# Performance work log

Hardware: AMD Instinct MI355X
Metric: run time of the kernel (lower is better)

## Reference

```python
import jax, jax.numpy as jnp
import numpy as np

K_WIN = 7  # temporal window size (odd)
EPS = 1e-5


def setup_inputs() -> dict:
    key = jax.random.key(0)
    ks = jax.random.split(key, 10)
    B, C, T, H, W = 8, 512, 32, 7, 7
    N, E = 8, 64  # heads, inter channels = C // N
    s = 0.02
    return {
        "x": jax.random.normal(ks[0], (B, C, T, H, W), jnp.float32),
        "gamma": jnp.ones((C,), jnp.float32),
        "beta": jnp.zeros((C,), jnp.float32),
        "Wq": jax.random.normal(ks[1], (N, E, C), jnp.float32) * s,
        "bq": jax.random.normal(ks[2], (N, E), jnp.float32) * s,
        "Wk": jax.random.normal(ks[3], (N, E, C), jnp.float32) * s,
        "bk": jax.random.normal(ks[4], (N, E), jnp.float32) * s,
        "Wv": jax.random.normal(ks[5], (N, E, C), jnp.float32) * s,
        "bv": jax.random.normal(ks[6], (N, E), jnp.float32) * s,
        "Wo": jax.random.normal(ks[7], (N, C, E), jnp.float32) * s,
        "bo": jax.random.normal(ks[8], (N, C), jnp.float32) * s,
    }


def reference(x, gamma, beta, Wq, bq, Wk, bk, Wv, bv, Wo, bo):
    B, C, T, H, W = x.shape
    K = K_WIN
    P = H * W          # spatial positions per frame
    L = K * P          # positions per temporal window

    # BatchNorm3d (training-mode batch stats over B,T,H,W)
    mean = jnp.mean(x, axis=(0, 2, 3, 4), keepdims=True)
    var = jnp.var(x, axis=(0, 2, 3, 4), keepdims=True)
    g = gamma[None, :, None, None, None]
    b = beta[None, :, None, None, None]
    xb = g * (x - mean) * jax.lax.rsqrt(var + EPS) + b  # (B,C,T,H,W)

    # temporal zero-pad so that number of windows S == T
    pad = K // 2
    xp = jnp.pad(xb, ((0, 0), (0, 0), (pad, pad), (0, 0), (0, 0)))
    # gather sliding windows: (B,C,T,K,H,W)
    win_idx = jnp.arange(T)[:, None] + jnp.arange(K)[None, :]
    xw = xp[:, :, win_idx]

    xwf = xw.reshape(B, C, T, L)   # window tokens (key/value source)
    xcf = xb.reshape(B, C, T, P)   # center frame (query source)

    # per-head projections (dropout is identity in eval mode)
    q = jnp.einsum('nec,bctp->bntep', Wq, xcf) + bq[None, :, None, :, None]
    k = jnp.einsum('nec,bctl->bntel', Wk, xwf) + bk[None, :, None, :, None]
    v = jnp.einsum('nec,bctl->bntel', Wv, xwf) + bv[None, :, None, :, None]

    # attention: scores (B,N,T,P,L), softmax over window positions L (no scaling, as in original)
    alpha = jnp.einsum('bntep,bntel->bntpl', q, k)
    alpha = jax.nn.softmax(alpha, axis=-1)
    y = jnp.einsum('bntpl,bntel->bntep', alpha, v)

    # output projection per head, then mean over heads
    out = jnp.einsum('nce,bntep->bntcp', Wo, y) + bo[None, :, None, :, None]
    z = jnp.mean(out, axis=1)                 # (B,T,C,P)
    z = jnp.transpose(z, (0, 2, 1, 3)).reshape(B, C, T, H, W)
    return z + xb  # residual with BN output
```

## Files before the change

kernel.cpp:

```cpp
#include <hip/hip_runtime.h>
#include <hip/hip_bf16.h>


typedef float f32x4 __attribute__((ext_vector_type(4)));
typedef short s16x8 __attribute__((ext_vector_type(8)));
typedef short s16x4 __attribute__((ext_vector_type(4)));
typedef __bf16 bf16x8 __attribute__((ext_vector_type(8)));

static __device__ __forceinline__ float bf2f(unsigned short u){
  union { unsigned int i; float f; } x; x.i = ((unsigned int)u) << 16; return x.f;
}
static __device__ __forceinline__ unsigned short f2bf(float f){
  union { __hip_bfloat16 h; unsigned short u; } x; x.h = __float2bfloat16(f); return x.u;
}
static __device__ __forceinline__ f32x4 mfma16(s16x8 a, s16x8 b, f32x4 c){
  return __builtin_amdgcn_mfma_f32_16x16x32_bf16(
      __builtin_bit_cast(bf16x8, a), __builtin_bit_cast(bf16x8, b), c, 0, 0, 0);
}
static __device__ __forceinline__ void gload16(const unsigned short* g, unsigned short* l){
  __builtin_amdgcn_global_load_lds(
      (const __attribute__((address_space(1))) unsigned int*)g,
      (__attribute__((address_space(3))) unsigned int*)l, 16, 0, 0);
}

__global__ __launch_bounds__(256) void stats_kernel(const float* __restrict__ x,
    const float* __restrict__ gamma, const float* __restrict__ beta,
    float* __restrict__ scale, float* __restrict__ shift){
  const int c = blockIdx.x, tid = threadIdx.x;
  float s1 = 0.f, s2 = 0.f;
  const float* xc = x + (size_t)c*1568;
  for (int i = tid; i < 3136; i += 256){
    int b = i / 392, j = i - b*392;
    f32x4 v = *(const f32x4*)(xc + (size_t)b*802816 + j*4);
    s1 += v[0]+v[1]+v[2]+v[3];
    s2 += v[0]*v[0]+v[1]*v[1]+v[2]*v[2]+v[3]*v[3];
  }
  #pragma unroll
  for (int off = 32; off > 0; off >>= 1){
    s1 += __shfl_down(s1, off);
    s2 += __shfl_down(s2, off);
  }
  __shared__ float r1[4], r2[4];
  int wave = tid >> 6, lane = tid & 63;
  if (lane == 0){ r1[wave] = s1; r2[wave] = s2; }
  __syncthreads();
  if (tid == 0){
    float t1 = r1[0]+r1[1]+r1[2]+r1[3];
    float t2 = r2[0]+r2[1]+r2[2]+r2[3];
    const float inv = 1.f/12544.f;
    float mean = t1*inv;
    float var  = t2*inv - mean*mean;
    float sc = gamma[c]*rsqrtf(var + 1e-5f);
    scale[c] = sc;
    shift[c] = beta[c] - mean*sc;
  }
}

__global__ __launch_bounds__(512) void pack_kernel(const float* __restrict__ Wq,
    const float* __restrict__ Wk, const float* __restrict__ Wv,
    const float* __restrict__ Wo, const float* __restrict__ bo,
    unsigned short* __restrict__ Wall, unsigned short* __restrict__ Wo2,
    float* __restrict__ bo_sum){
  int i = blockIdx.x*512 + threadIdx.x;
  if (i < 786432){
    const float* W = (i < 262144) ? Wq : (i < 524288 ? Wk : Wv);
    Wall[i] = f2bf(W[i & 262143]);
  } else if (i < 1048576){
    int j = i - 786432;
    int c = j >> 9, k = j & 511, nn = k >> 6, e = k & 63;
    Wo2[j] = f2bf(Wo[((size_t)nn*512 + c)*64 + e] * 0.125f);
  } else if (i < 1049088){
    int c = i - 1048576;
    float s = 0.f;
    #pragma unroll
    for (int nn = 0; nn < 8; ++nn) s += bo[nn*512 + c];
    bo_sum[c] = s * 0.125f;
  }
}

__global__ __launch_bounds__(256) void xt_kernel(const float* __restrict__ x,
    const float* __restrict__ scale, const float* __restrict__ shift,
    unsigned short* __restrict__ Xt){
  __shared__ unsigned short Xc[512][52];
  const int bt = blockIdx.x, b = bt >> 5, t = bt & 31, tid = threadIdx.x;
  const float* xb = x + (size_t)b*802816 + t*49;
  for (int i = tid; i < 512*49; i += 256){
    int c = i / 49, p = i - c*49;
    Xc[c][p] = f2bf(xb[(size_t)c*1568 + p]*scale[c] + shift[c]);
  }
  __syncthreads();
  unsigned short* dst = Xt + (size_t)bt*32768;
  for (int i = tid; i < 4096; i += 256){
    int p = i & 63, c0 = (i >> 6) << 3;
    s16x8 v;
    #pragma unroll
    for (int j = 0; j < 8; ++j) v[j] = (p < 49) ? (short)Xc[c0+j][p] : (short)0;
    *(s16x8*)(dst + p*512 + c0) = v;
  }
}

__global__ __launch_bounds__(256) void qkv_gemm(const unsigned short* __restrict__ Wall,
    const unsigned short* __restrict__ Xt,
    const float* __restrict__ bq, const float* __restrict__ bk, const float* __restrict__ bv,
    unsigned short* __restrict__ Qg, unsigned short* __restrict__ Kg,
    unsigned short* __restrict__ Vg){
  __shared__ unsigned short As[2][4096];
  __shared__ unsigned short Bs[2][4096];
  const int bid = blockIdx.x;
  const int id = (bid & 7)*192 + (bid >> 3);
  const int bm = id % 12, bn = id / 12;
  const int m0 = bm*128, n0 = bn*128;
  const int tid = threadIdx.x;
  const int w = __builtin_amdgcn_readfirstlane(tid >> 6);
  const int lane = tid & 63, l15 = lane & 15, g = lane >> 4, g4 = (lane >> 4)*4;
  const int wm = w >> 1, wn = w & 1;
  const int cA = w*128 + lane;
  int offA[4], offB[4];
  #pragma unroll
  for (int mi = 0; mi < 4; ++mi){
    int row = wm*64 + mi*16 + l15;
    offA[mi] = row*32 + ((g ^ ((row>>1)&3))<<3);
  }
  #pragma unroll
  for (int ni = 0; ni < 4; ++ni){
    int col = wn*64 + ni*16 + l15;
    offB[ni] = col*32 + ((g ^ ((col>>1)&3))<<3);
  }
  f32x4 acc[4][4];
  #pragma unroll
  for (int mi = 0; mi < 4; ++mi)
    #pragma unroll
    for (int ni = 0; ni < 4; ++ni) acc[mi][ni] = 0.f;

  auto stage = [&](int bufi, int ks){
    #pragma unroll
    for (int it = 0; it < 2; ++it){
      int c = cA + it*64;
      int row = c >> 2, slot = c & 3;
      int ko = ks*32 + ((slot ^ ((row>>1)&3))<<3);
      gload16(Wall + (size_t)(m0 + row)*512 + ko, &As[bufi][(w*128 + it*64)*8]);
      gload16(Xt   + (size_t)(n0 + row)*512 + ko, &Bs[bufi][(w*128 + it*64)*8]);
    }
  };
  auto compute = [&](int bufi){
    s16x8 Af[4], Bf[4];
    #pragma unroll
    for (int mi = 0; mi < 4; ++mi) Af[mi] = *(const s16x8*)&As[bufi][offA[mi]];
    #pragma unroll
    for (int ni = 0; ni < 4; ++ni) Bf[ni] = *(const s16x8*)&Bs[bufi][offB[ni]];
    #pragma unroll
    for (int mi = 0; mi < 4; ++mi)
      #pragma unroll
      for (int ni = 0; ni < 4; ++ni)
        acc[mi][ni] = mfma16(Af[mi], Bf[ni], acc[mi][ni]);
  };

  stage(0, 0);
  __syncthreads();
  #pragma unroll 1
  for (int kk = 0; kk < 8; ++kk){
    stage(1, kk*2 + 1);
    compute(0);
    __syncthreads();
    if (kk < 7) stage(0, kk*2 + 2);
    compute(1);
    __syncthreads();
  }

  const int qb = bm*2 + wm;
  const int which = qb >> 3, n = qb & 7;
  const int bt = bn*2 + wn, b = bt >> 5, t = bt & 31;
  const size_t bnt = ((size_t)(b*8 + n)*32 + t);
  const float* bias = which == 0 ? bq : (which == 1 ? bk : bv);
  #pragma unroll
  for (int mi = 0; mi < 4; ++mi){
    const int e0 = mi*16 + g4;
    const f32x4 bb = *(const f32x4*)(bias + n*64 + e0);
    #pragma unroll
    for (int ni = 0; ni < 4; ++ni){
      const int p = ni*16 + l15;
      f32x4 v = acc[mi][ni] + bb;
      if (which == 0) v *= 1.4426950408889634f;
      if (p < 49){
        if (which < 2){
          s16x4 u;
          #pragma unroll
          for (int r = 0; r < 4; ++r) u[r] = (short)f2bf(v[r]);
          *(s16x4*)((which == 0 ? Qg : Kg) + (bnt*49 + p)*64 + e0) = u;
        } else {
          #pragma unroll
          for (int r = 0; r < 4; ++r)
            Vg[bnt*3328 + (size_t)(e0 + r)*52 + p] = f2bf(v[r]);
        }
      }
    }
  }
}

__global__ __launch_bounds__(512,2) void attn_kernel(const unsigned short* __restrict__ Qg,
    const unsigned short* __restrict__ Kg, const unsigned short* __restrict__ Vg,
    const float* __restrict__ bk, const float* __restrict__ bv,
    unsigned short* __restrict__ Yg){
  const int bid = blockIdx.x;
  const int bt = ((bid & 7) << 5) | (bid >> 3);
  const int b = bt >> 5, t = bt & 31, tid = threadIdx.x;
  const int n = __builtin_amdgcn_readfirstlane(tid >> 6);
  const int lane = tid & 63, g = lane >> 4, l15 = lane & 15, g4 = (lane >> 4)*4;
  const size_t bnt = ((size_t)(b*8 + n)*32 + t);
  const unsigned short* Qb = Qg + bnt*3136;
  s16x8 Qf[4][2];
  #pragma unroll
  for (int ni = 0; ni < 4; ++ni)
    #pragma unroll
    for (int ks = 0; ks < 2; ++ks)
      Qf[ni][ks] = *(const s16x8*)(Qb + (ni*16 + l15)*64 + ks*32 + g*8);
  const float* bkp = bk + n*64;
  f32x4 bkf[2][2];
  bkf[0][0] = *(const f32x4*)(bkp + g*8);      bkf[0][1] = *(const f32x4*)(bkp + g*8 + 4);
  bkf[1][0] = *(const f32x4*)(bkp + 32 + g*8); bkf[1][1] = *(const f32x4*)(bkp + 32 + g*8 + 4);
  float pad_l[4];
  #pragma unroll
  for (int ni = 0; ni < 4; ++ni){
    float s = 0.f;
    #pragma unroll
    for (int ks = 0; ks < 2; ++ks)
      #pragma unroll
      for (int h = 0; h < 2; ++h)
        #pragma unroll
        for (int j = 0; j < 4; ++j)
          s += bf2f((unsigned short)Qf[ni][ks][h*4+j]) * bkf[ks][h][j];
    s += __shfl_xor(s, 16); s += __shfl_xor(s, 32);
    pad_l[ni] = s;
  }
  float m_run[4], d_run[4];
  f32x4 Yacc[4][4];
  #pragma unroll
  for (int ni = 0; ni < 4; ++ni){
    m_run[ni] = -1e30f; d_run[ni] = 0.f;
    #pragma unroll
    for (int me = 0; me < 4; ++me) Yacc[me][ni] = 0.f;
  }
  int slo = 3 - t; if (slo < 0) slo = 0;
  int shi = 34 - t; if (shi > 6) shi = 6;
  for (int s = slo; s <= shi; ++s){
    const int tt = t + s - 3;
    const unsigned short* Kb = Kg + ((size_t)(b*8 + n)*32 + tt)*3136;
    const unsigned short* Vb = Vg + ((size_t)(b*8 + n)*32 + tt)*3328;
    f32x4 S[4][4];
    #pragma unroll
    for (int mi = 0; mi < 4; ++mi)
      #pragma unroll
      for (int ni = 0; ni < 4; ++ni) S[mi][ni] = 0.f;
    __builtin_amdgcn_s_setprio(1);
    #pragma unroll
    for (int ks = 0; ks < 2; ++ks)
      #pragma unroll
      for (int mi = 0; mi < 4; ++mi){
        s16x8 Kf = *(const s16x8*)(Kb + (mi*16 + l15)*64 + ks*32 + g*8);
        #pragma unroll
        for (int ni = 0; ni < 4; ++ni)
          S[mi][ni] = mfma16(Kf, Qf[ni][ks], S[mi][ni]);
      }
    __builtin_amdgcn_s_setprio(0);
    #pragma unroll
    for (int r = 0; r < 4; ++r){
      const bool bad = (g4 + r) >= 1;
      #pragma unroll
      for (int ni = 0; ni < 4; ++ni)
        S[3][ni][r] = bad ? -1e30f : S[3][ni][r];
    }
    #pragma unroll
    for (int ni = 0; ni < 4; ++ni){
      float mx = -1e30f;
      #pragma unroll
      for (int mi = 0; mi < 4; ++mi)
        #pragma unroll
        for (int r = 0; r < 4; ++r) mx = fmaxf(mx, S[mi][ni][r]);
      mx = fmaxf(mx, __shfl_xor(mx, 16));
      mx = fmaxf(mx, __shfl_xor(mx, 32));
      const float mn = fmaxf(m_run[ni], mx);
      const float rs = exp2f(m_run[ni] - mn);
      m_run[ni] = mn;
      float sum = 0.f;
      #pragma unroll
      for (int mi = 0; mi < 4; ++mi)
        #pragma unroll
        for (int r = 0; r < 4; ++r){
          float e = exp2f(S[mi][ni][r] - mn);
          S[mi][ni][r] = e; sum += e;
        }
      sum += __shfl_xor(sum, 16); sum += __shfl_xor(sum, 32);
      d_run[ni] = d_run[ni]*rs + sum;
      #pragma unroll
      for (int me = 0; me < 4; ++me) Yacc[me][ni] *= rs;
    }
    #pragma unroll
    for (int ks = 0; ks < 2; ++ks){
      s16x8 Pf[4];
      #pragma unroll
      for (int ni = 0; ni < 4; ++ni){
        f32x4 a = S[2*ks][ni], b2 = S[2*ks+1][ni];
        s16x8 pf;
        #pragma unroll
        for (int j = 0; j < 4; ++j){
          pf[j]   = (short)f2bf(a[j]);
          pf[4+j] = (short)f2bf(b2[j]);
        }
        Pf[ni] = pf;
      }
      __builtin_amdgcn_s_setprio(1);
      #pragma unroll
      for (int me = 0; me < 4; ++me){
        s16x4 vlo = *(const s16x4*)(Vb + (size_t)(me*16 + l15)*52 + ks*32 + g4);
        s16x4 vhi = *(const s16x4*)(Vb + (size_t)(me*16 + l15)*52 + ks*32 + 16 + g4);
        s16x8 Vf;
        #pragma unroll
        for (int j = 0; j < 4; ++j){ Vf[j] = vlo[j]; Vf[4+j] = vhi[j]; }
        #pragma unroll
        for (int ni = 0; ni < 4; ++ni)
          Yacc[me][ni] = mfma16(Vf, Pf[ni], Yacc[me][ni]);
      }
      __builtin_amdgcn_s_setprio(0);
    }
  }
  const int n_pad = slo + (6 - shi);
  f32x4 bvf[4];
  #pragma unroll
  for (int me = 0; me < 4; ++me)
    bvf[me] = *(const f32x4*)(bv + n*64 + me*16 + g4);
  unsigned short* Yb = Yg + bnt*3136;
  #pragma unroll
  for (int ni = 0; ni < 4; ++ni){
    float rs = 1.f, pw = 0.f, d = d_run[ni];
    if (n_pad > 0){
      const float mf = fmaxf(m_run[ni], pad_l[ni]);
      rs = exp2f(m_run[ni] - mf);
      pw = (float)(n_pad*49) * exp2f(pad_l[ni] - mf);
      d = d_run[ni]*rs + pw;
    }
    const float inv = 1.f/d;
    const int p = ni*16 + l15;
    if (p < 49){
      #pragma unroll
      for (int me = 0; me < 4; ++me){
        s16x4 u;
        #pragma unroll
        for (int r = 0; r < 4; ++r)
          u[r] = (short)f2bf((Yacc[me][ni][r]*rs + pw*bvf[me][r])*inv);
        *(s16x4*)(Yb + (size_t)p*64 + me*16 + g4) = u;
      }
    }
  }
}

__global__ __launch_bounds__(256) void out_gemm(const unsigned short* __restrict__ Wo2,
    const unsigned short* __restrict__ Yg, const unsigned short* __restrict__ Xt,
    const float* __restrict__ scale, const float* __restrict__ shift,
    const float* __restrict__ bo_sum, float* __restrict__ out){
  __shared__ unsigned short As[2][4096];
  __shared__ unsigned short Bs[2][4096];
  const int bid = blockIdx.x;
  const int id = (bid & 7)*64 + (bid >> 3);
  const int bm = id % 4, bn = id / 4;
  const int m0 = bm*128, n0 = bn*128;
  const int tid = threadIdx.x;
  const int w = __builtin_amdgcn_readfirstlane(tid >> 6);
  const int lane = tid & 63, l15 = lane & 15, g = lane >> 4, g4 = (lane >> 4)*4;
  const int wm = w >> 1, wn = w & 1;
  const int cA = w*128 + lane;
  int offA[4], offB[4];
  #pragma unroll
  for (int mi = 0; mi < 4; ++mi){
    int row = wm*64 + mi*16 + l15;
    offA[mi] = row*32 + ((g ^ ((row>>1)&3))<<3);
  }
  #pragma unroll
  for (int ni = 0; ni < 4; ++ni){
    int col = wn*64 + ni*16 + l15;
    offB[ni] = col*32 + ((g ^ ((col>>1)&3))<<3);
  }
  f32x4 acc[4][4];
  #pragma unroll
  for (int mi = 0; mi < 4; ++mi)
    #pragma unroll
    for (int ni = 0; ni < 4; ++ni) acc[mi][ni] = 0.f;

  auto stage = [&](int bufi, int ks){
    const int nh = ks >> 1, eo = (ks & 1)*32;
    #pragma unroll
    for (int it = 0; it < 2; ++it){
      int c = cA + it*64;
      int row = c >> 2, slot = c & 3;
      int sw = ((slot ^ ((row>>1)&3))<<3);
      gload16(Wo2 + (size_t)(m0 + row)*512 + ks*32 + sw, &As[bufi][(w*128 + it*64)*8]);
      const int col = n0 + row, btc = col >> 6, p = col & 63;
      const size_t bb = ((size_t)((btc >> 5)*8 + nh)*32 + (btc & 31));
      gload16(Yg + bb*3136 + p*64 + eo + sw, &Bs[bufi][(w*128 + it*64)*8]);
    }
  };
  auto compute = [&](int bufi){
    s16x8 Af[4], Bf[4];
    #pragma unroll
    for (int mi = 0; mi < 4; ++mi) Af[mi] = *(const s16x8*)&As[bufi][offA[mi]];
    #pragma unroll
    for (int ni = 0; ni < 4; ++ni) Bf[ni] = *(const s16x8*)&Bs[bufi][offB[ni]];
    #pragma unroll
    for (int mi = 0; mi < 4; ++mi)
      #pragma unroll
      for (int ni = 0; ni < 4; ++ni)
        acc[mi][ni] = mfma16(Af[mi], Bf[ni], acc[mi][ni]);
  };

  stage(0, 0);
  __syncthreads();
  #pragma unroll 1
  for (int kk = 0; kk < 8; ++kk){
    stage(1, kk*2 + 1);
    compute(0);
    __syncthreads();
    if (kk < 7) stage(0, kk*2 + 2);
    compute(1);
    __syncthreads();
  }

  const int cb = m0 + wm*64;
  const int bt = bn*2 + wn, b = bt >> 5, t = bt & 31;
  const unsigned short* XtB = Xt + (size_t)bt*32768;
  #pragma unroll
  for (int mi = 0; mi < 4; ++mi){
    const int c0 = cb + mi*16 + g4;
    const f32x4 sc = *(const f32x4*)(bo_sum + c0);
    #pragma unroll
    for (int ni = 0; ni < 4; ++ni){
      const int p = ni*16 + l15;
      if (p < 49){
        s16x4 xb = *(const s16x4*)(XtB + p*512 + c0);
        #pragma unroll
        for (int r = 0; r < 4; ++r){
          const int c = c0 + r;
          out[((size_t)(b*512 + c))*1568 + t*49 + p] =
              acc[mi][ni][r] + sc[r] + bf2f((unsigned short)xb[r]);
        }
      }
    }
  }
}

extern "C" void kernel_launch(void* const* d_in, const int* in_sizes, int n_in_,
                              void* d_out, int out_size, void* d_ws, size_t ws_size,
                              hipStream_t stream){
  const float* x     = (const float*)d_in[0];
  const float* gamma = (const float*)d_in[1];
  const float* beta  = (const float*)d_in[2];
  const float* Wq    = (const float*)d_in[3];
  const float* bq    = (const float*)d_in[4];
  const float* Wk    = (const float*)d_in[5];
  const float* bk    = (const float*)d_in[6];
  const float* Wv    = (const float*)d_in[7];
  const float* bv    = (const float*)d_in[8];
  const float* Wo    = (const float*)d_in[9];
  const float* bo    = (const float*)d_in[10];
  float* out = (float*)d_out;

  char* ws = (char*)d_ws;
  float* scale  = (float*)ws;
  float* shift  = scale + 512;
  float* bo_sum = shift + 512;
  unsigned short* Wall = (unsigned short*)(ws + 8192);
  const size_t PAD = 16384;
  unsigned short* Wo2 = Wall + 786432;
  unsigned short* Xt  = Wo2 + 262144;
  unsigned short* Qg  = Xt + 8388608;
  unsigned short* Kg  = Qg + 6422528 + PAD;
  unsigned short* Vg  = Kg + 6422528 + PAD;
  unsigned short* Yg  = Vg + 6815744 + PAD;

  hipLaunchKernelGGL(stats_kernel, dim3(512), dim3(256), 0, stream,
                     x, gamma, beta, scale, shift);
  hipLaunchKernelGGL(pack_kernel, dim3(2049), dim3(512), 0, stream,
                     Wq, Wk, Wv, Wo, bo, Wall, Wo2, bo_sum);
  hipLaunchKernelGGL(xt_kernel, dim3(256), dim3(256), 0, stream,
                     x, scale, shift, Xt);
  hipLaunchKernelGGL(qkv_gemm, dim3(1536), dim3(256), 0, stream,
                     Wall, Xt, bq, bk, bv, Qg, Kg, Vg);
  hipLaunchKernelGGL(attn_kernel, dim3(256), dim3(512), 0, stream,
                     Qg, Kg, Vg, bk, bv, Yg);
  hipLaunchKernelGGL(out_gemm, dim3(512), dim3(256), 0, stream,
                     Wo2, Yg, Xt, scale, shift, bo_sum, out);
}
```

Measured before the change: 128.4 us.

## Deepen GEMM LDS pipeline to four stages with vmcnt-based waits

Both the QKV and output-projection GEMMs move from a double-buffered LDS pipeline synchronised by __syncthreads to a four-buffer ring. The ring prefetches three k-steps ahead and waits with explicit s_waitcnt vmcnt plus a raw s_barrier, so global loads stay in flight across iterations instead of being drained every step. The compute phase also runs under raised wave priority. In exchange LDS use per block doubles to 64 KB, which may cut occupancy, and the hand-counted vmcnt values must match the number of loads issued per stage.

```diff
diff --git a/kernel.cpp b/kernel.cpp
--- a/kernel.cpp
+++ b/kernel.cpp
@@ -22,6 +22,7 @@
       (const __attribute__((address_space(1))) unsigned int*)g,
       (__attribute__((address_space(3))) unsigned int*)l, 16, 0, 0);
 }
+#define VMCNT(N) asm volatile("s_waitcnt vmcnt(" #N ")" ::: "memory")
 
 __global__ __launch_bounds__(256) void stats_kernel(const float* __restrict__ x,
     const float* __restrict__ gamma, const float* __restrict__ beta,
@@ -104,8 +105,8 @@
     const float* __restrict__ bq, const float* __restrict__ bk, const float* __restrict__ bv,
     unsigned short* __restrict__ Qg, unsigned short* __restrict__ Kg,
     unsigned short* __restrict__ Vg){
-  __shared__ unsigned short As[2][4096];
-  __shared__ unsigned short Bs[2][4096];
+  __shared__ unsigned short As[4][4096];
+  __shared__ unsigned short Bs[4][4096];
   const int bid = blockIdx.x;
   const int id = (bid & 7)*192 + (bid >> 3);
   const int bm = id % 12, bn = id / 12;
@@ -155,17 +156,23 @@
         acc[mi][ni] = mfma16(Af[mi], Bf[ni], acc[mi][ni]);
   };
 
-  stage(0, 0);
-  __syncthreads();
+  stage(0, 0); stage(1, 1); stage(2, 2);
   #pragma unroll 1
-  for (int kk = 0; kk < 8; ++kk){
-    stage(1, kk*2 + 1);
-    compute(0);
-    __syncthreads();
-    if (kk < 7) stage(0, kk*2 + 2);
-    compute(1);
-    __syncthreads();
-  }
+  for (int j = 0; j < 13; ++j){
+    VMCNT(8);
+    __builtin_amdgcn_s_barrier();
+    __builtin_amdgcn_sched_barrier(0);
+    stage((j+3) & 3, j+3);
+    __builtin_amdgcn_s_setprio(1);
+    compute(j & 3);
+    __builtin_amdgcn_s_setprio(0);
+  }
+  VMCNT(8);  __builtin_amdgcn_s_barrier(); __builtin_amdgcn_sched_barrier(0);
+  __builtin_amdgcn_s_setprio(1); compute(1); __builtin_amdgcn_s_setprio(0);
+  VMCNT(4);  __builtin_amdgcn_s_barrier(); __builtin_amdgcn_sched_barrier(0);
+  __builtin_amdgcn_s_setprio(1); compute(2); __builtin_amdgcn_s_setprio(0);
+  VMCNT(0);  __builtin_amdgcn_s_barrier(); __builtin_amdgcn_sched_barrier(0);
+  __builtin_amdgcn_s_setprio(1); compute(3); __builtin_amdgcn_s_setprio(0);
 
   const int qb = bm*2 + wm;
   const int which = qb >> 3, n = qb & 7;
@@ -357,8 +364,8 @@
     const unsigned short* __restrict__ Yg, const unsigned short* __restrict__ Xt,
     const float* __restrict__ scale, const float* __restrict__ shift,
     const float* __restrict__ bo_sum, float* __restrict__ out){
-  __shared__ unsigned short As[2][4096];
-  __shared__ unsigned short Bs[2][4096];
+  __shared__ unsigned short As[4][4096];
+  __shared__ unsigned short Bs[4][4096];
   const int bid = blockIdx.x;
   const int id = (bid & 7)*64 + (bid >> 3);
   const int bm = id % 4, bn = id / 4;
@@ -411,17 +418,23 @@
         acc[mi][ni] = mfma16(Af[mi], Bf[ni], acc[mi][ni]);
   };
 
-  stage(0, 0);
-  __syncthreads();
+  stage(0, 0); stage(1, 1); stage(2, 2);
   #pragma unroll 1
-  for (int kk = 0; kk < 8; ++kk){
-    stage(1, kk*2 + 1);
-    compute(0);
-    __syncthreads();
-    if (kk < 7) stage(0, kk*2 + 2);
-    compute(1);
-    __syncthreads();
-  }
+  for (int j = 0; j < 13; ++j){
+    VMCNT(8);
+    __builtin_amdgcn_s_barrier();
+    __builtin_amdgcn_sched_barrier(0);
+    stage((j+3) & 3, j+3);
+    __builtin_amdgcn_s_setprio(1);
+    compute(j & 3);
+    __builtin_amdgcn_s_setprio(0);
+  }
+  VMCNT(8);  __builtin_amdgcn_s_barrier(); __builtin_amdgcn_sched_barrier(0);
+  __builtin_amdgcn_s_setprio(1); compute(1); __builtin_amdgcn_s_setprio(0);
+  VMCNT(4);  __builtin_amdgcn_s_barrier(); __builtin_amdgcn_sched_barrier(0);
+  __builtin_amdgcn_s_setprio(1); compute(2); __builtin_amdgcn_s_setprio(0);
+  VMCNT(0);  __builtin_amdgcn_s_barrier(); __builtin_amdgcn_sched_barrier(0);
+  __builtin_amdgcn_s_setprio(1); compute(3); __builtin_amdgcn_s_setprio(0);
 
   const int cb = m0 + wm*64;
   const int bt = bn*2 + wn, b = bt >> 5, t = bt & 31;
```

Result: no change. 130.7 us (+1.7%).

## Fold BatchNorm into QKV weights and pack tokens densely without padding

Applied to the files above, without the earlier changes.

Raw x is now transposed to bf16 once, and the BN statistics are computed from that bf16 copy in a two-pass reduction instead of a strided read of x. The BN scale is folded into the QKV weights and the shift into per-row biases, and the normalized residual is rebuilt in the out_gemm epilogue. Token columns are packed densely (49 per frame instead of padded to 64), which shrinks the QKV and output GEMM grids and removes wasted MFMA work. This adds two small kernels and computes the statistics from bf16-rounded values, a slight change in precision.

```diff
diff --git a/kernel.cpp b/kernel.cpp
--- a/kernel.cpp
+++ b/kernel.cpp
@@ -3,6 +3,7 @@
 
 
 typedef float f32x4 __attribute__((ext_vector_type(4)));
+typedef float f32x2 __attribute__((ext_vector_type(2)));
 typedef short s16x8 __attribute__((ext_vector_type(8)));
 typedef short s16x4 __attribute__((ext_vector_type(4)));
 typedef __bf16 bf16x8 __attribute__((ext_vector_type(8)));
@@ -23,48 +24,80 @@
       (__attribute__((address_space(3))) unsigned int*)l, 16, 0, 0);
 }
 
-__global__ __launch_bounds__(256) void stats_kernel(const float* __restrict__ x,
+__global__ __launch_bounds__(256) void xt_kernel(const float* __restrict__ x,
+    unsigned short* __restrict__ Xt){
+  __shared__ unsigned short Xc[512][53];
+  const int bt = blockIdx.x, b = bt >> 5, t = bt & 31, tid = threadIdx.x;
+  const float* xb = x + (size_t)b*802816 + t*49;
+  for (int i = tid; i < 512*49; i += 256){
+    int c = i / 49, p = i - c*49;
+    Xc[c][p] = f2bf(xb[(size_t)c*1568 + p]);
+  }
+  __syncthreads();
+  unsigned short* dst = Xt + (size_t)bt*49*512;
+  for (int i = tid; i < 49*64; i += 256){
+    int p = i >> 6, c0 = (i & 63) << 3;
+    s16x8 v;
+    #pragma unroll
+    for (int j = 0; j < 8; ++j) v[j] = (short)Xc[c0+j][p];
+    *(s16x8*)(dst + p*512 + c0) = v;
+  }
+}
+
+__global__ __launch_bounds__(256) void stats1_kernel(const unsigned short* __restrict__ Xt,
+    float* __restrict__ partials){
+  __shared__ float R1[4][512];
+  __shared__ float R2[4][512];
+  const int blk = blockIdx.x, tid = threadIdx.x;
+  const int rt = tid >> 6, c0 = (tid & 63)*8;
+  const int r0 = blk*128;
+  float s1[8] = {0,0,0,0,0,0,0,0}, s2[8] = {0,0,0,0,0,0,0,0};
+  for (int r = rt; r < 128; r += 4){
+    s16x8 v = *(const s16x8*)(Xt + (size_t)(r0 + r)*512 + c0);
+    #pragma unroll
+    for (int j = 0; j < 8; ++j){
+      float f = bf2f((unsigned short)v[j]);
+      s1[j] += f; s2[j] += f*f;
+    }
+  }
+  #pragma unroll
+  for (int j = 0; j < 8; ++j){ R1[rt][c0+j] = s1[j]; R2[rt][c0+j] = s2[j]; }
+  __syncthreads();
+  for (int c = tid; c < 512; c += 256){
+    f32x2 o;
+    o[0] = R1[0][c]+R1[1][c]+R1[2][c]+R1[3][c];
+    o[1] = R2[0][c]+R2[1][c]+R2[2][c]+R2[3][c];
+    *(f32x2*)(partials + ((size_t)blk*512 + c)*2) = o;
+  }
+}
+
+__global__ __launch_bounds__(512) void stats2_kernel(const float* __restrict__ partials,
     const float* __restrict__ gamma, const float* __restrict__ beta,
     float* __restrict__ scale, float* __restrict__ shift){
-  const int c = blockIdx.x, tid = threadIdx.x;
+  const int c = threadIdx.x;
   float s1 = 0.f, s2 = 0.f;
-  const float* xc = x + (size_t)c*1568;
-  for (int i = tid; i < 3136; i += 256){
-    int b = i / 392, j = i - b*392;
-    f32x4 v = *(const f32x4*)(xc + (size_t)b*802816 + j*4);
-    s1 += v[0]+v[1]+v[2]+v[3];
-    s2 += v[0]*v[0]+v[1]*v[1]+v[2]*v[2]+v[3]*v[3];
-  }
-  #pragma unroll
-  for (int off = 32; off > 0; off >>= 1){
-    s1 += __shfl_down(s1, off);
-    s2 += __shfl_down(s2, off);
-  }
-  __shared__ float r1[4], r2[4];
-  int wave = tid >> 6, lane = tid & 63;
-  if (lane == 0){ r1[wave] = s1; r2[wave] = s2; }
-  __syncthreads();
-  if (tid == 0){
-    float t1 = r1[0]+r1[1]+r1[2]+r1[3];
-    float t2 = r2[0]+r2[1]+r2[2]+r2[3];
-    const float inv = 1.f/12544.f;
-    float mean = t1*inv;
-    float var  = t2*inv - mean*mean;
-    float sc = gamma[c]*rsqrtf(var + 1e-5f);
-    scale[c] = sc;
-    shift[c] = beta[c] - mean*sc;
-  }
+  for (int k = 0; k < 98; ++k){
+    f32x2 v = *(const f32x2*)(partials + ((size_t)k*512 + c)*2);
+    s1 += v[0]; s2 += v[1];
+  }
+  const float inv = 1.f/12544.f;
+  float mean = s1*inv;
+  float var  = s2*inv - mean*mean;
+  float sc = gamma[c]*rsqrtf(var + 1e-5f);
+  scale[c] = sc;
+  shift[c] = beta[c] - mean*sc;
 }
 
 __global__ __launch_bounds__(512) void pack_kernel(const float* __restrict__ Wq,
     const float* __restrict__ Wk, const float* __restrict__ Wv,
     const float* __restrict__ Wo, const float* __restrict__ bo,
+    const float* __restrict__ scale,
     unsigned short* __restrict__ Wall, unsigned short* __restrict__ Wo2,
     float* __restrict__ bo_sum){
   int i = blockIdx.x*512 + threadIdx.x;
   if (i < 786432){
     const float* W = (i < 262144) ? Wq : (i < 524288 ? Wk : Wv);
-    Wall[i] = f2bf(W[i & 262143]);
+    Wall[i] = f2bf(W[i & 262143] * scale[i & 511]);
   } else if (i < 1048576){
     int j = i - 786432;
     int c = j >> 9, k = j & 511, nn = k >> 6, e = k & 63;
@@ -78,36 +111,32 @@
   }
 }
 
-__global__ __launch_bounds__(256) void xt_kernel(const float* __restrict__ x,
-    const float* __restrict__ scale, const float* __restrict__ shift,
-    unsigned short* __restrict__ Xt){
-  __shared__ unsigned short Xc[512][52];
-  const int bt = blockIdx.x, b = bt >> 5, t = bt & 31, tid = threadIdx.x;
-  const float* xb = x + (size_t)b*802816 + t*49;
-  for (int i = tid; i < 512*49; i += 256){
-    int c = i / 49, p = i - c*49;
-    Xc[c][p] = f2bf(xb[(size_t)c*1568 + p]*scale[c] + shift[c]);
-  }
-  __syncthreads();
-  unsigned short* dst = Xt + (size_t)bt*32768;
-  for (int i = tid; i < 4096; i += 256){
-    int p = i & 63, c0 = (i >> 6) << 3;
-    s16x8 v;
-    #pragma unroll
-    for (int j = 0; j < 8; ++j) v[j] = (p < 49) ? (short)Xc[c0+j][p] : (short)0;
-    *(s16x8*)(dst + p*512 + c0) = v;
-  }
+__global__ __launch_bounds__(64) void bias_kernel(const float* __restrict__ Wq,
+    const float* __restrict__ Wk, const float* __restrict__ Wv,
+    const float* __restrict__ bq, const float* __restrict__ bk,
+    const float* __restrict__ bv, const float* __restrict__ shift,
+    float* __restrict__ biasAll){
+  const int row = blockIdx.x, lane = threadIdx.x;
+  const float* W    = row < 512 ? Wq : (row < 1024 ? Wk : Wv);
+  const float* bsrc = row < 512 ? bq : (row < 1024 ? bk : bv);
+  const int r = row & 511;
+  const float* Wr = W + (size_t)r*512;
+  float s = 0.f;
+  #pragma unroll
+  for (int j = 0; j < 8; ++j) s += Wr[lane + 64*j]*shift[lane + 64*j];
+  #pragma unroll
+  for (int off = 32; off > 0; off >>= 1) s += __shfl_down(s, off);
+  if (lane == 0) biasAll[row] = bsrc[r] + s;
 }
 
 __global__ __launch_bounds__(256) void qkv_gemm(const unsigned short* __restrict__ Wall,
-    const unsigned short* __restrict__ Xt,
-    const float* __restrict__ bq, const float* __restrict__ bk, const float* __restrict__ bv,
+    const unsigned short* __restrict__ Xt, const float* __restrict__ biasAll,
     unsigned short* __restrict__ Qg, unsigned short* __restrict__ Kg,
     unsigned short* __restrict__ Vg){
   __shared__ unsigned short As[2][4096];
   __shared__ unsigned short Bs[2][4096];
   const int bid = blockIdx.x;
-  const int id = (bid & 7)*192 + (bid >> 3);
+  const int id = (bid & 7)*147 + (bid >> 3);
   const int bm = id % 12, bn = id / 12;
   const int m0 = bm*128, n0 = bn*128;
   const int tid = threadIdx.x;
@@ -169,29 +198,29 @@
 
   const int qb = bm*2 + wm;
   const int which = qb >> 3, n = qb & 7;
-  const int bt = bn*2 + wn, b = bt >> 5, t = bt & 31;
-  const size_t bnt = ((size_t)(b*8 + n)*32 + t);
-  const float* bias = which == 0 ? bq : (which == 1 ? bk : bv);
-  #pragma unroll
-  for (int mi = 0; mi < 4; ++mi){
-    const int e0 = mi*16 + g4;
-    const f32x4 bb = *(const f32x4*)(bias + n*64 + e0);
-    #pragma unroll
-    for (int ni = 0; ni < 4; ++ni){
-      const int p = ni*16 + l15;
-      f32x4 v = acc[mi][ni] + bb;
+  f32x4 bb[4];
+  #pragma unroll
+  for (int mi = 0; mi < 4; ++mi)
+    bb[mi] = *(const f32x4*)(biasAll + qb*64 + mi*16 + g4);
+  #pragma unroll
+  for (int ni = 0; ni < 4; ++ni){
+    const int col = n0 + wn*64 + ni*16 + l15;
+    const int btc = col / 49, p = col - btc*49;
+    const size_t bnt = ((size_t)((btc >> 5)*8 + n)*32 + (btc & 31));
+    #pragma unroll
+    for (int mi = 0; mi < 4; ++mi){
+      const int e0 = mi*16 + g4;
+      f32x4 v = acc[mi][ni] + bb[mi];
       if (which == 0) v *= 1.4426950408889634f;
-      if (p < 49){
-        if (which < 2){
-          s16x4 u;
-          #pragma unroll
-          for (int r = 0; r < 4; ++r) u[r] = (short)f2bf(v[r]);
-          *(s16x4*)((which == 0 ? Qg : Kg) + (bnt*49 + p)*64 + e0) = u;
-        } else {
-          #pragma unroll
-          for (int r = 0; r < 4; ++r)
-            Vg[bnt*3328 + (size_t)(e0 + r)*52 + p] = f2bf(v[r]);
-        }
+      if (which < 2){
+        s16x4 u;
+        #pragma unroll
+        for (int r = 0; r < 4; ++r) u[r] = (short)f2bf(v[r]);
+        *(s16x4*)((which == 0 ? Qg : Kg) + (bnt*49 + p)*64 + e0) = u;
+      } else {
+        #pragma unroll
+        for (int r = 0; r < 4; ++r)
+          Vg[bnt*3328 + (size_t)(e0 + r)*52 + p] = f2bf(v[r]);
       }
     }
   }
@@ -360,7 +389,7 @@
   __shared__ unsigned short As[2][4096];
   __shared__ unsigned short Bs[2][4096];
   const int bid = blockIdx.x;
-  const int id = (bid & 7)*64 + (bid >> 3);
+  const int id = (bid & 7)*49 + (bid >> 3);
   const int bm = id % 4, bn = id / 4;
   const int m0 = bm*128, n0 = bn*128;
   const int tid = threadIdx.x;
@@ -393,7 +422,8 @@
       int row = c >> 2, slot = c & 3;
       int sw = ((slot ^ ((row>>1)&3))<<3);
       gload16(Wo2 + (size_t)(m0 + row)*512 + ks*32 + sw, &As[bufi][(w*128 + it*64)*8]);
-      const int col = n0 + row, btc = col >> 6, p = col & 63;
+      const int col = n0 + row;
+      const int btc = col / 49, p = col - btc*49;
       const size_t bb = ((size_t)((btc >> 5)*8 + nh)*32 + (btc & 31));
       gload16(Yg + bb*3136 + p*64 + eo + sw, &Bs[bufi][(w*128 + it*64)*8]);
     }
@@ -424,23 +454,28 @@
   }
 
   const int cb = m0 + wm*64;
-  const int bt = bn*2 + wn, b = bt >> 5, t = bt & 31;
-  const unsigned short* XtB = Xt + (size_t)bt*32768;
+  int colv[4]; size_t obase[4];
+  #pragma unroll
+  for (int ni = 0; ni < 4; ++ni){
+    const int col = n0 + wn*64 + ni*16 + l15;
+    const int btc = col / 49, p = col - btc*49;
+    const int b = btc >> 5, t = btc & 31;
+    colv[ni] = col;
+    obase[ni] = (size_t)b*802816 + t*49 + p;
+  }
   #pragma unroll
   for (int mi = 0; mi < 4; ++mi){
     const int c0 = cb + mi*16 + g4;
-    const f32x4 sc = *(const f32x4*)(bo_sum + c0);
+    const f32x4 bs = *(const f32x4*)(bo_sum + c0);
+    const f32x4 sc = *(const f32x4*)(scale + c0);
+    const f32x4 sh = *(const f32x4*)(shift + c0);
     #pragma unroll
     for (int ni = 0; ni < 4; ++ni){
-      const int p = ni*16 + l15;
-      if (p < 49){
-        s16x4 xb = *(const s16x4*)(XtB + p*512 + c0);
-        #pragma unroll
-        for (int r = 0; r < 4; ++r){
-          const int c = c0 + r;
-          out[((size_t)(b*512 + c))*1568 + t*49 + p] =
-              acc[mi][ni][r] + sc[r] + bf2f((unsigned short)xb[r]);
-        }
+      s16x4 xb = *(const s16x4*)(Xt + (size_t)colv[ni]*512 + c0);
+      #pragma unroll
+      for (int r = 0; r < 4; ++r){
+        out[obase[ni] + (size_t)(c0 + r)*1568] =
+            acc[mi][ni][r] + bs[r] + sc[r]*bf2f((unsigned short)xb[r]) + sh[r];
       }
     }
   }
@@ -463,28 +498,32 @@
   float* out = (float*)d_out;
 
   char* ws = (char*)d_ws;
-  float* scale  = (float*)ws;
-  float* shift  = scale + 512;
-  float* bo_sum = shift + 512;
-  unsigned short* Wall = (unsigned short*)(ws + 8192);
+  float* scale    = (float*)ws;
+  float* shift    = scale + 512;
+  float* bo_sum   = shift + 512;
+  float* biasAll  = bo_sum + 512;
+  float* partials = biasAll + 1536;
+  unsigned short* Wall = (unsigned short*)(ws + 417792);
   const size_t PAD = 16384;
   unsigned short* Wo2 = Wall + 786432;
   unsigned short* Xt  = Wo2 + 262144;
-  unsigned short* Qg  = Xt + 8388608;
+  unsigned short* Qg  = Xt + 6422528;
   unsigned short* Kg  = Qg + 6422528 + PAD;
   unsigned short* Vg  = Kg + 6422528 + PAD;
   unsigned short* Yg  = Vg + 6815744 + PAD;
 
-  hipLaunchKernelGGL(stats_kernel, dim3(512), dim3(256), 0, stream,
-                     x, gamma, beta, scale, shift);
+  hipLaunchKernelGGL(xt_kernel, dim3(256), dim3(256), 0, stream, x, Xt);
+  hipLaunchKernelGGL(stats1_kernel, dim3(98), dim3(256), 0, stream, Xt, partials);
+  hipLaunchKernelGGL(stats2_kernel, dim3(1), dim3(512), 0, stream,
+                     partials, gamma, beta, scale, shift);
   hipLaunchKernelGGL(pack_kernel, dim3(2049), dim3(512), 0, stream,
-                     Wq, Wk, Wv, Wo, bo, Wall, Wo2, bo_sum);
-  hipLaunchKernelGGL(xt_kernel, dim3(256), dim3(256), 0, stream,
-                     x, scale, shift, Xt);
-  hipLaunchKernelGGL(qkv_gemm, dim3(1536), dim3(256), 0, stream,
-                     Wall, Xt, bq, bk, bv, Qg, Kg, Vg);
+                     Wq, Wk, Wv, Wo, bo, scale, Wall, Wo2, bo_sum);
+  hipLaunchKernelGGL(bias_kernel, dim3(1536), dim3(64), 0, stream,
+                     Wq, Wk, Wv, bq, bk, bv, shift, biasAll);
+  hipLaunchKernelGGL(qkv_gemm, dim3(1176), dim3(256), 0, stream,
+                     Wall, Xt, biasAll, Qg, Kg, Vg);
   hipLaunchKernelGGL(attn_kernel, dim3(256), dim3(512), 0, stream,
                      Qg, Kg, Vg, bk, bv, Yg);
-  hipLaunchKernelGGL(out_gemm, dim3(512), dim3(256), 0, stream,
+  hipLaunchKernelGGL(out_gemm, dim3(392), dim3(256), 0, stream,
                      Wo2, Yg, Xt, scale, shift, bo_sum, out);
 }
```

Result: slower. 137.1 us (+6.7%).
